# Kernel optimization log

Measured on AMD Instinct MI355X. Metric: run time of the kernel, lower is better.

Reference implementation:

```python
import jax, jax.numpy as jnp
import numpy as np

N = 50000       # nodes
E = 800000      # edges (before self loops)
F_IN = 128      # feat_dim
H = 8           # heads
C = 64          # hidden_dim (per-head out_channels, averaged since concat=False)
G = 64          # graphs in batch
NEG_SLOPE = 0.2


def setup_inputs() -> dict:
    key = jax.random.key(0)
    ks = jax.random.split(key, 16)
    inp = {
        "x": jax.random.normal(ks[0], (N, F_IN), jnp.float32),
        "edge_index": jax.random.randint(ks[1], (2, E), 0, N, dtype=jnp.int32),
        "batch": jnp.sort(jax.random.randint(ks[2], (N,), 0, G, dtype=jnp.int32)),
        "edge_attr": jax.random.normal(ks[3], (E, 4), jnp.float32),
    }
    # GATConv params per layer: lin weight [in, H*C], att_src/att_dst [H, C], bias [C]
    dims_in = [F_IN, C, C]
    for i, din in enumerate(dims_in):
        s = 1.0 / np.sqrt(din)
        inp[f"W{i}"] = jax.random.uniform(ks[4 + 3 * i], (din, H * C), jnp.float32, -s, s)
        inp[f"asrc{i}"] = jax.random.uniform(ks[5 + 3 * i], (H, C), jnp.float32, -s, s)
        inp[f"adst{i}"] = jax.random.uniform(ks[6 + 3 * i], (H, C), jnp.float32, -s, s)
        inp[f"b{i}"] = jnp.zeros((C,), jnp.float32)
    return inp


def _gat_conv(x, src, dst, W, asrc, adst, b):
    n = x.shape[0]
    h = (x @ W).reshape(n, H, C)                       # [N,H,C]
    a_s = (h * asrc[None]).sum(-1)                     # [N,H]
    a_d = (h * adst[None]).sum(-1)                     # [N,H]
    e = a_s[src] + a_d[dst]                            # [Etot,H]
    e = jnp.where(e > 0, e, NEG_SLOPE * e)             # leaky_relu(0.2)
    # segment softmax over incoming edges of each dst node (self loops => nonempty)
    m = jax.ops.segment_max(e, dst, num_segments=n)    # [N,H]
    ex = jnp.exp(e - m[dst])
    denom = jax.ops.segment_sum(ex, dst, num_segments=n)
    alpha = ex / denom[dst]                            # [Etot,H]
    out = jax.ops.segment_sum(alpha[:, :, None] * h[src], dst, num_segments=n)  # [N,H,C]
    return out.mean(axis=1) + b[None]                  # concat=False -> head mean, + bias


def reference(x, edge_index, batch, edge_attr,
              W0, asrc0, adst0, b0,
              W1, asrc1, adst1, b1,
              W2, asrc2, adst2, b2):
    # edge_attr is ignored: GATConv built without edge_dim has no lin_edge.
    loop = jnp.arange(N, dtype=edge_index.dtype)
    src = jnp.concatenate([edge_index[0], loop])       # PyG add_self_loops=True
    dst = jnp.concatenate([edge_index[1], loop])
    layers = [(W0, asrc0, adst0, b0), (W1, asrc1, adst1, b1), (W2, asrc2, adst2, b2)]
    xs = []
    h = x
    for (W, a_s, a_d, b) in layers:
        h = jax.nn.elu(_gat_conv(h, src, dst, W, a_s, a_d, b))
        xs.append(h)
    # pool='sum' -> global_add_pool per layer, then concat over layers
    pooled = [jax.ops.segment_sum(t, batch, num_segments=G) for t in xs]
    global_rep = jnp.concatenate(pooled, axis=1)       # [G, 3*C]
    return global_rep, h
```

## Files before the change

kernel.cpp:

```cpp
#include <hip/hip_runtime.h>
#include <math.h>

#define NN 50000
#define EE 800000
#define ET (EE + NN)
#define FIN 128
#define HH 8
#define CC 64
#define HC 512
#define HU 256
#define GG 64
#define POOL_SZ (GG * 3 * CC)

typedef short short8 __attribute__((ext_vector_type(8)));
typedef float floatx4 __attribute__((ext_vector_type(4)));

__device__ __forceinline__ unsigned bf16pack(float a, float b) {
    unsigned ua = __float_as_uint(a), ub = __float_as_uint(b);
    ua = (ua + 0x7FFFu + ((ua >> 16) & 1u)) >> 16;
    ub = (ub + 0x7FFFu + ((ub >> 16) & 1u)) >> 16;
    return ua | (ub << 16);
}
__device__ __forceinline__ unsigned short bf16r(float a) {
    unsigned ua = __float_as_uint(a);
    return (unsigned short)((ua + 0x7FFFu + ((ua >> 16) & 1u)) >> 16);
}
__device__ __forceinline__ float bf_lo(unsigned u) { return __uint_as_float(u << 16); }
__device__ __forceinline__ float bf_hi(unsigned u) { return __uint_as_float(u & 0xFFFF0000u); }


__global__ void k_prep(const float* __restrict__ in, unsigned* __restrict__ out, int* cnt) {
    int i = blockIdx.x * blockDim.x + threadIdx.x;
    if (i < NN * FIN / 8) {
        float4 a = ((const float4*)in)[i * 2];
        float4 b = ((const float4*)in)[i * 2 + 1];
        uint4 o;
        o.x = bf16pack(a.x, a.y); o.y = bf16pack(a.z, a.w);
        o.z = bf16pack(b.x, b.y); o.w = bf16pack(b.z, b.w);
        ((uint4*)out)[i] = o;
    }
    if (i < NN) cnt[i] = 1;
}


__global__ void k_count(const int* __restrict__ dst, int* cnt) {
    int e = blockIdx.x * blockDim.x + threadIdx.x;
    if (e < EE) atomicAdd(&cnt[dst[e]], 1);
}

__global__ __launch_bounds__(1024) void k_scanall(
        const int* __restrict__ cnt, int* __restrict__ off,
        int* __restrict__ cursor, int* __restrict__ col) {
    __shared__ int s[1024];
    const int t = threadIdx.x;
    const int CPT = (NN + 1023) / 1024;
    int base = t * CPT;
    int lim = NN - base;
    if (lim < 0) lim = 0;
    if (lim > CPT) lim = CPT;
    int sum = 0;
    for (int i = 0; i < lim; ++i) sum += cnt[base + i];
    s[t] = sum;
    __syncthreads();
    for (int d = 1; d < 1024; d <<= 1) {
        int v = (t >= d) ? s[t - d] : 0;
        __syncthreads();
        s[t] += v;
        __syncthreads();
    }
    int run = s[t] - sum;
    for (int i = 0; i < lim; ++i) {
        int c = cnt[base + i];
        off[base + i] = run;
        cursor[base + i] = run + 1;
        col[run] = base + i;
        run += c;
    }
    if (t == 0) off[NN] = ET;
}

__global__ void k_fill(const int* __restrict__ src, const int* __restrict__ dst,
                       int* cursor, int* col) {
    int e = blockIdx.x * blockDim.x + threadIdx.x;
    if (e < EE) {
        int p = atomicAdd(&cursor[dst[e]], 1);
        col[p] = src[e];
    }
}


template<int K>
__global__ __launch_bounds__(256) void k_gemm_mfma(
        const unsigned short* __restrict__ A,
        const float* __restrict__ W,
        const float* __restrict__ asrc, const float* __restrict__ adst,
        unsigned short* __restrict__ hout,
        float* __restrict__ as_out, float* __restrict__ ad_out, int M) {
    __shared__ unsigned short Asl[4][64][8];
    __shared__ unsigned short Bsl[4][64][8];
    const int row0 = blockIdx.x * 64;
    const int head = blockIdx.y;
    const int col0 = head * 64;
    const int tid  = threadIdx.x;
    const int w    = tid >> 6;
    const int lane = tid & 63;
    const int kgl  = lane >> 4;
    const int l15  = lane & 15;

    floatx4 acc[4] = {};

    const int kgs = tid >> 6;
    const int rc  = tid & 63;

    for (int kt = 0; kt < K; kt += 32) {
        uint4 av = make_uint4(0, 0, 0, 0);
        if (row0 + rc < M)
            av = *(const uint4*)(A + (size_t)(row0 + rc) * K + kt + kgs * 8);
        *(uint4*)&Asl[kgs][rc][0] = av;
        float wv[8];
        #pragma unroll
        for (int e = 0; e < 8; ++e)
            wv[e] = W[(size_t)(kt + kgs * 8 + e) * HC + col0 + rc];
        uint4 bv;
        bv.x = bf16pack(wv[0], wv[1]); bv.y = bf16pack(wv[2], wv[3]);
        bv.z = bf16pack(wv[4], wv[5]); bv.w = bf16pack(wv[6], wv[7]);
        *(uint4*)&Bsl[kgs][rc][0] = bv;
        __syncthreads();

        short8 af = *(const short8*)&Asl[kgl][16 * w + l15][0];
        #pragma unroll
        for (int fj = 0; fj < 4; ++fj) {
            short8 bf = *(const short8*)&Bsl[kgl][16 * fj + l15][0];
            acc[fj] = __builtin_amdgcn_mfma_f32_16x16x32_bf16(af, bf, acc[fj], 0, 0, 0);
        }
        __syncthreads();
    }

    float sav[4], dav[4];
    #pragma unroll
    for (int fj = 0; fj < 4; ++fj) {
        sav[fj] = asrc[col0 + 16 * fj + l15];
        dav[fj] = adst[col0 + 16 * fj + l15];
    }
    const int r4 = lane >> 4;
    #pragma unroll
    for (int reg = 0; reg < 4; ++reg) {
        int gr = row0 + 16 * w + r4 * 4 + reg;
        float ps = acc[0][reg] * sav[0] + acc[1][reg] * sav[1]
                 + acc[2][reg] * sav[2] + acc[3][reg] * sav[3];
        float pd = acc[0][reg] * dav[0] + acc[1][reg] * dav[1]
                 + acc[2][reg] * dav[2] + acc[3][reg] * dav[3];
        ps += __shfl_xor(ps, 1); ps += __shfl_xor(ps, 2);
        ps += __shfl_xor(ps, 4); ps += __shfl_xor(ps, 8);
        pd += __shfl_xor(pd, 1); pd += __shfl_xor(pd, 2);
        pd += __shfl_xor(pd, 4); pd += __shfl_xor(pd, 8);
        if (gr < M) {
            #pragma unroll
            for (int fj = 0; fj < 4; ++fj)
                hout[(size_t)gr * HC + col0 + 16 * fj + l15] = bf16r(acc[fj][reg]);
            if (l15 == 0) {
                as_out[gr * HH + head] = ps;
                ad_out[gr * HH + head] = pd;
            }
        }
    }
}


__global__ __launch_bounds__(256) void k_aggw(
        const unsigned* __restrict__ hb, const float* __restrict__ as,
        const float* __restrict__ ad, const int* __restrict__ off,
        const int* __restrict__ col, const float* __restrict__ bias,
        float* __restrict__ yout, unsigned* __restrict__ yb) {
    __shared__ float s_alpha[2][2][64][4];
    __shared__ int   s_src[2][2][64];
    __shared__ float2 s_red[2][32];

    const int wv   = (threadIdx.x >> 6) & 1;
    const int nd   = threadIdx.x >> 7;
    const int lane = threadIdx.x & 63;
    const int n    = blockIdx.x * 2 + nd;
    const int e0   = off[n];
    const int tot  = off[n + 1] - e0;
    const int hsel = lane >> 5;

    float4 adv = *(const float4*)&ad[n * HH + 4 * wv];

    float d0 = 0.f, d1 = 0.f;
    float acc[4] = {0.f, 0.f, 0.f, 0.f};

    for (int base = 0; base < tot; base += 64) {
        const int cnt = min(64, tot - base);
        float n0, n1, n2, n3;
        if (lane < cnt) {
            int s = col[e0 + base + lane];
            s_src[nd][wv][lane] = s;
            float4 a = *(const float4*)&as[s * HH + 4 * wv];
            float e0v = a.x + adv.x, e1v = a.y + adv.y;
            float e2v = a.z + adv.z, e3v = a.w + adv.w;
            e0v = e0v > 0.f ? e0v : 0.2f * e0v;
            e1v = e1v > 0.f ? e1v : 0.2f * e1v;
            e2v = e2v > 0.f ? e2v : 0.2f * e2v;
            e3v = e3v > 0.f ? e3v : 0.2f * e3v;
            n0 = __expf(e0v); n1 = __expf(e1v);
            n2 = __expf(e2v); n3 = __expf(e3v);
            *(float4*)&s_alpha[nd][wv][lane][0] = make_float4(n0, n1, n2, n3);
        } else {
            n0 = n1 = n2 = n3 = 0.f;
        }
        #define RED(v) { v += __shfl_xor(v, 1);  v += __shfl_xor(v, 2); \
                         v += __shfl_xor(v, 4);  v += __shfl_xor(v, 8); \
                         v += __shfl_xor(v, 16); v += __shfl_xor(v, 32); }
        RED(n0); RED(n1); RED(n2); RED(n3);
        #undef RED
        d0 += hsel ? n1 : n0;
        d1 += hsel ? n3 : n2;
        #define STEP(jj) { \
            int sj = s_src[nd][wv][jj]; \
            const unsigned* _p = &hb[(size_t)sj * HU + wv * 128 + lane]; \
            unsigned u0 = _p[0], u1 = _p[64]; \
            float a0 = s_alpha[nd][wv][jj][hsel]; \
            float a1 = s_alpha[nd][wv][jj][2 + hsel]; \
            acc[0] += a0 * bf_lo(u0); acc[1] += a0 * bf_hi(u0); \
            acc[2] += a1 * bf_lo(u1); acc[3] += a1 * bf_hi(u1); }
        int j = 0;
        for (; j + 4 <= cnt; j += 4) { STEP(j); STEP(j + 1); STEP(j + 2); STEP(j + 3); }
        for (; j < cnt; ++j) STEP(j);
        #undef STEP
    }

    float r0 = 1.f / d0, r1 = 1.f / d1;
    float sx = acc[0] * r0 + acc[2] * r1;
    float sy = acc[1] * r0 + acc[3] * r1;
    sx += __shfl_xor(sx, 32);
    sy += __shfl_xor(sy, 32);
    if (wv == 1 && lane < 32) s_red[nd][lane] = make_float2(sx, sy);
    __syncthreads();
    if (wv == 0 && lane < 32) {
        float2 o = s_red[nd][lane];
        float2 bv = *(const float2*)&bias[lane * 2];
        float vx = (sx + o.x) * 0.125f + bv.x;
        float vy = (sy + o.y) * 0.125f + bv.y;
        vx = vx > 0.f ? vx : (__expf(vx) - 1.f);
        vy = vy > 0.f ? vy : (__expf(vy) - 1.f);
        *(float2*)&yout[(size_t)n * CC + lane * 2] = make_float2(vx, vy);
        yb[(size_t)n * 32 + lane] = bf16pack(vx, vy);
    }
}


__global__ __launch_bounds__(256) void k_pool(
        const float* __restrict__ y, const int* __restrict__ batch,
        float* __restrict__ pooled, int layerOff) {
    __shared__ float red[256];
    const int g = blockIdx.x;
    const int t = threadIdx.x;
    int lo = 0, hi = NN;
    while (lo < hi) { int mid = (lo + hi) >> 1; if (batch[mid] < g) lo = mid + 1; else hi = mid; }
    const int nlo = lo;
    lo = nlo; hi = NN;
    while (lo < hi) { int mid = (lo + hi) >> 1; if (batch[mid] < g + 1) lo = mid + 1; else hi = mid; }
    const int nhi = lo;

    const int c = t & 63, r = t >> 6;
    float sum = 0.f;
    for (int n = nlo + r; n < nhi; n += 4) sum += y[(size_t)n * CC + c];
    red[t] = sum;
    __syncthreads();
    if (t < 64)
        pooled[g * (3 * CC) + layerOff + t] = red[t] + red[t + 64] + red[t + 128] + red[t + 192];
}


extern "C" void kernel_launch(void* const* d_in, const int* in_sizes, int n_in,
                              void* d_out, int out_size, void* d_ws, size_t ws_size,
                              hipStream_t stream) {
    const float* x      = (const float*)d_in[0];
    const int*   ei     = (const int*)d_in[1];
    const int*   batch  = (const int*)d_in[2];
    const float* W0     = (const float*)d_in[4];
    const float* asrc0  = (const float*)d_in[5];
    const float* adst0  = (const float*)d_in[6];
    const float* b0     = (const float*)d_in[7];
    const float* W1     = (const float*)d_in[8];
    const float* asrc1  = (const float*)d_in[9];
    const float* adst1  = (const float*)d_in[10];
    const float* b1     = (const float*)d_in[11];
    const float* W2     = (const float*)d_in[12];
    const float* asrc2  = (const float*)d_in[13];
    const float* adst2  = (const float*)d_in[14];
    const float* b2     = (const float*)d_in[15];

    const int* src = ei;
    const int* dst = ei + EE;

    float* outp   = (float*)d_out;
    float* pooled = outp;
    float* hfinal = outp + POOL_SZ;

    unsigned* hb     = (unsigned*)d_ws;
    float*    y      = (float*)(hb + (size_t)NN * HU);
    float*    as_buf = y + (size_t)NN * CC;
    float*    ad_buf = as_buf + (size_t)NN * HH;
    unsigned* xb     = (unsigned*)(ad_buf + (size_t)NN * HH);
    unsigned* yb     = xb + (size_t)NN * 64;
    int*      off    = (int*)(yb + (size_t)NN * 32);
    int*      cursor = off + (NN + 1);
    int*      cnt    = cursor + NN;
    int*      col    = cnt + NN;

    k_prep<<<(NN * FIN / 8 + 255) / 256, 256, 0, stream>>>(x, xb, cnt);
    k_count<<<(EE + 255) / 256, 256, 0, stream>>>(dst, cnt);
    k_scanall<<<1, 1024, 0, stream>>>(cnt, off, cursor, col);
    k_fill<<<(EE + 255) / 256, 256, 0, stream>>>(src, dst, cursor, col);

    dim3 ggrid((NN + 63) / 64, HH);

    const float* Ws_[3]  = {W0, W1, W2};
    const float* sa_[3]  = {asrc0, asrc1, asrc2};
    const float* da_[3]  = {adst0, adst1, adst2};
    const float* bb_[3]  = {b0, b1, b2};
    float* youts[3] = {y, y, hfinal};

    for (int L = 0; L < 3; ++L) {
        if (L == 0)
            k_gemm_mfma<FIN><<<ggrid, 256, 0, stream>>>(
                (const unsigned short*)xb, Ws_[0], sa_[0], da_[0],
                (unsigned short*)hb, as_buf, ad_buf, NN);
        else
            k_gemm_mfma<CC><<<ggrid, 256, 0, stream>>>(
                (const unsigned short*)yb, Ws_[L], sa_[L], da_[L],
                (unsigned short*)hb, as_buf, ad_buf, NN);
        k_aggw<<<NN / 2, 256, 0, stream>>>(hb, as_buf, ad_buf, off, col,
                                           bb_[L], youts[L], yb);
        k_pool<<<GG, 256, 0, stream>>>(youts[L], batch, pooled, L * CC);
    }
}
```

Measured before the change: 959.2 us.

## Replace single-block CSR offset scan with three-pass multi-block scan

The exclusive prefix scan over per-node in-degree counts used to run in one 1024-thread block, with each thread walking about 49 elements serially and making strided, uncoalesced loads and stores. It is now a three-kernel scan: per-block scans of 256 elements, a single-block scan of the 196 block totals, and a fixup pass that adds block offsets and writes off, cursor and the self-loop column entries with coalesced accesses. This spreads the scan over the whole GPU but costs two extra kernel launches. It also needs a block-sum buffer placed after col in the workspace, which assumes the workspace has room for it.

```diff
diff --git a/kernel.cpp b/kernel.cpp
--- a/kernel.cpp
+++ b/kernel.cpp
@@ -48,35 +48,47 @@
     if (e < EE) atomicAdd(&cnt[dst[e]], 1);
 }
 
-__global__ __launch_bounds__(1024) void k_scanall(
-        const int* __restrict__ cnt, int* __restrict__ off,
-        int* __restrict__ cursor, int* __restrict__ col) {
-    __shared__ int s[1024];
-    const int t = threadIdx.x;
-    const int CPT = (NN + 1023) / 1024;
-    int base = t * CPT;
-    int lim = NN - base;
-    if (lim < 0) lim = 0;
-    if (lim > CPT) lim = CPT;
-    int sum = 0;
-    for (int i = 0; i < lim; ++i) sum += cnt[base + i];
-    s[t] = sum;
+#define SCAN_B 256
+__global__ void k_scan1(const int* __restrict__ cnt, int* off, int* bsum, int n) {
+    __shared__ int s[SCAN_B];
+    int i = blockIdx.x * SCAN_B + threadIdx.x;
+    int v = (i < n) ? cnt[i] : 0;
+    s[threadIdx.x] = v;
     __syncthreads();
-    for (int d = 1; d < 1024; d <<= 1) {
-        int v = (t >= d) ? s[t - d] : 0;
-        __syncthreads();
-        s[t] += v;
-        __syncthreads();
-    }
-    int run = s[t] - sum;
-    for (int i = 0; i < lim; ++i) {
-        int c = cnt[base + i];
-        off[base + i] = run;
-        cursor[base + i] = run + 1;
-        col[run] = base + i;
-        run += c;
-    }
-    if (t == 0) off[NN] = ET;
+    for (int d = 1; d < SCAN_B; d <<= 1) {
+        int t = (threadIdx.x >= d) ? s[threadIdx.x - d] : 0;
+        __syncthreads();
+        s[threadIdx.x] += t;
+        __syncthreads();
+    }
+    if (i < n) off[i] = s[threadIdx.x] - v;
+    if (threadIdx.x == SCAN_B - 1) bsum[blockIdx.x] = s[SCAN_B - 1];
+}
+
+__global__ void k_scan2(int* bsum, int nb) {
+    __shared__ int s[SCAN_B];
+    int v = (threadIdx.x < nb) ? bsum[threadIdx.x] : 0;
+    s[threadIdx.x] = v;
+    __syncthreads();
+    for (int d = 1; d < SCAN_B; d <<= 1) {
+        int t = (threadIdx.x >= d) ? s[threadIdx.x - d] : 0;
+        __syncthreads();
+        s[threadIdx.x] += t;
+        __syncthreads();
+    }
+    if (threadIdx.x < nb) bsum[threadIdx.x] = s[threadIdx.x] - v;
+}
+
+__global__ void k_scan3(int* off, const int* __restrict__ bsum, int* cursor,
+                        int* __restrict__ col, int n, int total) {
+    int i = blockIdx.x * blockDim.x + threadIdx.x;
+    if (i < n) {
+        int v = off[i] + bsum[i / SCAN_B];
+        off[i] = v;
+        cursor[i] = v + 1;
+        col[v] = i;
+    }
+    if (i == 0) off[n] = total;
 }
 
 __global__ void k_fill(const int* __restrict__ src, const int* __restrict__ dst,
@@ -308,10 +320,15 @@
     int*      cursor = off + (NN + 1);
     int*      cnt    = cursor + NN;
     int*      col    = cnt + NN;
+    int*      bsum   = col + ET;
+
+    const int NB = (NN + SCAN_B - 1) / SCAN_B;
 
     k_prep<<<(NN * FIN / 8 + 255) / 256, 256, 0, stream>>>(x, xb, cnt);
     k_count<<<(EE + 255) / 256, 256, 0, stream>>>(dst, cnt);
-    k_scanall<<<1, 1024, 0, stream>>>(cnt, off, cursor, col);
+    k_scan1<<<NB, SCAN_B, 0, stream>>>(cnt, off, bsum, NN);
+    k_scan2<<<1, SCAN_B, 0, stream>>>(bsum, NB);
+    k_scan3<<<(NN + 255) / 256, 256, 0, stream>>>(off, bsum, cursor, col, NN, ET);
     k_fill<<<(EE + 255) / 256, 256, 0, stream>>>(src, dst, cursor, col);
 
     dim3 ggrid((NN + 63) / 64, HH);
```

Measured after the change: 833.8 us. 1.15x faster.
